# Performance work log

Measured on AMD Instinct MI355X. Metric: run time of the kernel, lower is better.

Reference implementation:

```python
import math
import jax, jax.numpy as jnp
import numpy as np

N_QUBITS = 16
BATCH = 128
N_STATE = 2 ** N_QUBITS


def cnot_ring(n_qubits):
    """Permutation equivalent to a CNOT ring (faithful copy of the torch repo's numpy code)."""
    n2 = np.array([0, 2, 3, 1])
    if n_qubits == 2:
        return n2
    evens = np.zeros(2 ** (n_qubits - 1))
    answer = n2[::2]
    for i in range(1, n_qubits - 1):
        evens[:2 ** i] = answer
        a, b = np.array_split(answer, 2)
        evens[2 ** i:2 ** i + 2 ** (i - 1)] = a + 3 * 2 ** i
        evens[2 ** i + 2 ** (i - 1):2 ** (i + 1)] = b + 2 ** i
        answer = evens[:2 ** (i + 1)]
    a, b = np.split(evens.copy() + 2 ** (n_qubits - 2), 2)
    a = np.mod(a, 2 ** (n_qubits - 1))
    b, c = np.split(b, 2)
    b = b - 2 ** (n_qubits - 1)
    odds = np.concatenate((a, b, c), axis=0)[::-1]
    output = np.zeros(2 ** n_qubits)
    output[::2] = evens
    output[1::2] = odds
    return output.astype(int)


def binary_mask(n_qubits):
    """[n, 2**n] matrix; row i is bit (n-1-i from LSB) of the column index,
    matching torch binary_matrix (dim 0 of the [2]*n tensor is the MSB)."""
    idx = jnp.arange(2 ** n_qubits, dtype=jnp.int32)
    shifts = (n_qubits - 1 - jnp.arange(n_qubits, dtype=jnp.int32))
    return ((idx[None, :] >> shifts[:, None]) & 1).astype(jnp.float32)


def wht(x):
    """Walsh-Hadamard transform over the last dim of [B, N] complex state (had_big butterfly)."""
    B, N = x.shape
    n = int(math.log2(N))
    for i in range(n):
        x = x.reshape(B, 2 ** i, 2, N >> (i + 1))
        a, b = x[:, :, 0, :], x[:, :, 1, :]
        x = jnp.stack([a + b, a - b], axis=2)
    return x.reshape(B, N) * jnp.asarray(2.0 ** (-n / 2), dtype=x.dtype)


def setup_inputs() -> dict:
    key = jax.random.key(0)
    k1, k2, k3 = jax.random.split(key, 3)
    state_re = jax.random.normal(k1, (BATCH, N_STATE), dtype=jnp.float32)
    state_im = jax.random.normal(k2, (BATCH, N_STATE), dtype=jnp.float32)
    thetas = jax.random.normal(k3, (BATCH, N_QUBITS), dtype=jnp.float32)
    cnot_p = jnp.asarray(cnot_ring(N_QUBITS), dtype=jnp.int32)
    return {"state_re": state_re, "state_im": state_im, "thetas": thetas, "cnot_p": cnot_p}


def reference(state_re, state_im, thetas, cnot_p):
    # set_state('random'): l2-normalize complex state per batch row
    norm = jnp.sqrt(jnp.sum(state_re * state_re + state_im * state_im, axis=-1, keepdims=True))
    state = (state_re + 1j * state_im) / norm  # complex64 [B, N]
    # hadamard layer (had_big WHT butterfly)
    state = wht(state)
    # RZ layer: thetas @ binary mask -> phase eigenvalues exp(-i*theta/2)
    ang = thetas @ binary_mask(N_QUBITS)  # [B, N]
    state = state * jnp.exp(-0.5j * ang)
    # CNOT ring: gather permutation over the state axis
    state = state[:, cnot_p]
    # second hadamard layer
    state = wht(state)
    # measure(): probabilities |psi|^2
    return jnp.abs(state) ** 2
```

## Files before the change

kernel.cpp:

```cpp
#include <hip/hip_runtime.h>

#define NB 128
#define NS 65536

template <int CTRL>
__device__ __forceinline__ float dppqp(float x) {
  return __int_as_float(__builtin_amdgcn_update_dpp(
      0, __float_as_int(x), CTRL, 0xF, 0xF, false));
}
template <int OFF>
__device__ __forceinline__ float dswz(float x) {
  return __int_as_float(__builtin_amdgcn_ds_swizzle(__float_as_int(x), OFF));
}

__device__ __forceinline__ void wht256(float (&xr)[4], float (&xi)[4], int lane) {
  {
    float t;
    t = xr[0]; xr[0] = t + xr[1]; xr[1] = t - xr[1];
    t = xr[2]; xr[2] = t + xr[3]; xr[3] = t - xr[3];
    t = xi[0]; xi[0] = t + xi[1]; xi[1] = t - xi[1];
    t = xi[2]; xi[2] = t + xi[3]; xi[3] = t - xi[3];
    t = xr[0]; xr[0] = t + xr[2]; xr[2] = t - xr[2];
    t = xr[1]; xr[1] = t + xr[3]; xr[3] = t - xr[3];
    t = xi[0]; xi[0] = t + xi[2]; xi[2] = t - xi[2];
    t = xi[1]; xi[1] = t + xi[3]; xi[3] = t - xi[3];
  }
  const float s1  = (lane & 1)  ? -1.f : 1.f;
  const float s2  = (lane & 2)  ? -1.f : 1.f;
  const float s4  = (lane & 4)  ? -1.f : 1.f;
  const float s8  = (lane & 8)  ? -1.f : 1.f;
  const float s16 = (lane & 16) ? -1.f : 1.f;
  const float s32 = (lane & 32) ? -1.f : 1.f;
#pragma unroll
  for (int q = 0; q < 4; ++q) {
    xr[q] = fmaf(s1, xr[q], dppqp<0xB1>(xr[q]));
    xi[q] = fmaf(s1, xi[q], dppqp<0xB1>(xi[q]));
  }
#pragma unroll
  for (int q = 0; q < 4; ++q) {
    xr[q] = fmaf(s2, xr[q], dppqp<0x4E>(xr[q]));
    xi[q] = fmaf(s2, xi[q], dppqp<0x4E>(xi[q]));
  }
#pragma unroll
  for (int q = 0; q < 4; ++q) {
    xr[q] = fmaf(s4, xr[q], dswz<0x101F>(xr[q]));
    xi[q] = fmaf(s4, xi[q], dswz<0x101F>(xi[q]));
  }
#pragma unroll
  for (int q = 0; q < 4; ++q) {
    xr[q] = fmaf(s8, xr[q], dswz<0x201F>(xr[q]));
    xi[q] = fmaf(s8, xi[q], dswz<0x201F>(xi[q]));
  }
#pragma unroll
  for (int q = 0; q < 4; ++q) {
    {
      auto r = __builtin_amdgcn_permlane16_swap(__float_as_uint(xr[q]),
                                                __float_as_uint(xr[q]), false, false);
      xr[q] = fmaf(s16, __uint_as_float(r[1]), __uint_as_float(r[0]));
    }
    {
      auto r = __builtin_amdgcn_permlane16_swap(__float_as_uint(xi[q]),
                                                __float_as_uint(xi[q]), false, false);
      xi[q] = fmaf(s16, __uint_as_float(r[1]), __uint_as_float(r[0]));
    }
  }
#pragma unroll
  for (int q = 0; q < 4; ++q) {
    {
      auto r = __builtin_amdgcn_permlane32_swap(__float_as_uint(xr[q]),
                                                __float_as_uint(xr[q]), false, false);
      xr[q] = fmaf(s32, __uint_as_float(r[1]), __uint_as_float(r[0]));
    }
    {
      auto r = __builtin_amdgcn_permlane32_swap(__float_as_uint(xi[q]),
                                                __float_as_uint(xi[q]), false, false);
      xi[q] = fmaf(s32, __uint_as_float(r[1]), __uint_as_float(r[0]));
    }
  }
}

__global__ __launch_bounds__(1024, 8) void k1_ahi(const float* __restrict__ sre,
                                                  const float* __restrict__ sim,
                                                  const float* __restrict__ thetas,
                                                  float* __restrict__ T,
                                                  float* __restrict__ partial) {
  __shared__ float sr[32][260];
  __shared__ float si[32][260];
  __shared__ float2 phh4[64];
  __shared__ float2 phHQ[4];
  __shared__ float th[16];
  __shared__ float red[16];
  const int bid = blockIdx.x;
  const int b = bid >> 3, tile = bid & 7;
  const int lo0 = tile * 32;
  const int tid = threadIdx.x, lane = tid & 63, w = tid >> 6;
  if (tid < 16) th[tid] = thetas[b * 16 + tid];
  __syncthreads();
  if (tid < 64) {
    float a = 0.f;
#pragma unroll
    for (int i = 0; i < 6; ++i)
      if ((tid >> (5 - i)) & 1) a += th[i];
    phh4[tid] = make_float2(cosf(0.5f * a), -sinf(0.5f * a));
    if (tid < 4) {
      float aq = 0.f;
      if (tid & 1) aq += th[7];
      if (tid & 2) aq += th[6];
      phHQ[tid] = make_float2(cosf(0.5f * aq), -sinf(0.5f * aq));
    }
  }
  const float* pre = sre + ((size_t)b << 16);
  const float* pim = sim + ((size_t)b << 16);
  float acc = 0.f;
  const int c = tid & 7, jr = tid >> 3;
#pragma unroll
  for (int it = 0; it < 2; ++it) {
    const int j = jr + it * 128;
    const float4 vr = *reinterpret_cast<const float4*>(pre + j * 256 + lo0 + c * 4);
    const float4 vi = *reinterpret_cast<const float4*>(pim + j * 256 + lo0 + c * 4);
    acc += vr.x*vr.x + vr.y*vr.y + vr.z*vr.z + vr.w*vr.w
         + vi.x*vi.x + vi.y*vi.y + vi.z*vi.z + vi.w*vi.w;
    sr[c*4+0][j] = vr.x; sr[c*4+1][j] = vr.y; sr[c*4+2][j] = vr.z; sr[c*4+3][j] = vr.w;
    si[c*4+0][j] = vi.x; si[c*4+1][j] = vi.y; si[c*4+2][j] = vi.z; si[c*4+3][j] = vi.w;
  }
#pragma unroll
  for (int m = 32; m >= 1; m >>= 1) acc += __shfl_xor(acc, m, 64);
  if (lane == 0) red[w] = acc;
  __syncthreads();
  if (tid == 0) {
    float sm = 0.f;
#pragma unroll
    for (int k = 0; k < 16; ++k) sm += red[k];
    partial[bid] = sm;
  }
#pragma unroll
  for (int r = 0; r < 2; ++r) {
    const int ll = w * 2 + r;
    const float4 a4 = *reinterpret_cast<const float4*>(&sr[ll][lane * 4]);
    const float4 b4 = *reinterpret_cast<const float4*>(&si[ll][lane * 4]);
    float xr[4] = {a4.x, a4.y, a4.z, a4.w};
    float xi[4] = {b4.x, b4.y, b4.z, b4.w};
    wht256(xr, xi, lane);
    const float2 p4 = phh4[lane];
#pragma unroll
    for (int q = 0; q < 4; ++q) {
      const float2 pq = phHQ[q];
      const float pr = p4.x * pq.x - p4.y * pq.y;
      const float pi = p4.x * pq.y + p4.y * pq.x;
      const float ur = xr[q], ui = xi[q];
      xr[q] = ur * pr - ui * pi;
      xi[q] = ur * pi + ui * pr;
    }
    wht256(xr, xi, lane);
    *reinterpret_cast<float4*>(&sr[ll][lane * 4]) = make_float4(xr[0], xr[1], xr[2], xr[3]);
    *reinterpret_cast<float4*>(&si[ll][lane * 4]) = make_float4(xi[0], xi[1], xi[2], xi[3]);
  }
  __syncthreads();
  float* Tb = T + ((size_t)b << 17);
  const int m = tid >> 2, sub = tid & 3;
  float* dst = Tb + ((size_t)m << 9) + (size_t)lo0 * 2;
#pragma unroll
  for (int j = 0; j < 4; ++j) {
    const int l0 = 8 * j + 2 * sub;
    *reinterpret_cast<float4*>(dst + l0 * 2) =
        make_float4(sr[l0][m], si[l0][m], sr[l0 + 1][m], si[l0 + 1][m]);
  }
}

__global__ __launch_bounds__(256, 8) void k2_alo_scatter(const float* __restrict__ T,
                                                         const float* __restrict__ thetas,
                                                         const int* __restrict__ cnot,
                                                         const float* __restrict__ partial,
                                                         float* __restrict__ outp) {
  __shared__ float2 phl4[64];
  __shared__ float2 phLQ[4];
  __shared__ int sloL[64];
  __shared__ int tj[16];
  __shared__ int srow16[16];
  __shared__ float th[16];
  __shared__ float shinv;
  const int bid = blockIdx.x;
  const int x = bid & 7, s2 = bid >> 3;
  const int b = x * 16 + (s2 >> 4), tile = s2 & 15;
  const int tid = threadIdx.x, lane = tid & 63, w = tid >> 6;
  if (tid < 16) {
    th[tid] = thetas[b * 16 + tid];
    int v = 0;
#pragma unroll
    for (int i = 0; i < 16; ++i) v |= ((cnot[1 << i] >> tid) & 1) << i;
    tj[tid] = v;
  }
  if (tid == 0) {
    float sum = 0.f;
#pragma unroll
    for (int k = 0; k < 8; ++k) sum += partial[b * 8 + k];
    shinv = 1.0f / (sum * 4294967296.0f);
  }
  __syncthreads();
  if (tid < 64) {
    float a = 0.f;
#pragma unroll
    for (int i = 0; i < 6; ++i)
      if ((tid >> (5 - i)) & 1) a += th[8 + i];
    phl4[tid] = make_float2(cosf(0.5f * a), -sinf(0.5f * a));
    int v = 0;
#pragma unroll
    for (int bb = 0; bb < 6; ++bb)
      if ((tid >> bb) & 1) v ^= tj[2 + bb];
    sloL[tid] = v;
    if (tid < 4) {
      float aq = 0.f;
      if (tid & 1) aq += th[15];
      if (tid & 2) aq += th[14];
      phLQ[tid] = make_float2(cosf(0.5f * aq), -sinf(0.5f * aq));
    }
  }
  if (tid < 16) {
    const int mh = tile * 16 + tid;
    int v = 0;
#pragma unroll
    for (int bb = 0; bb < 8; ++bb)
      if ((mh >> bb) & 1) v ^= tj[8 + bb];
    srow16[tid] = v;
  }
  __syncthreads();
  const float* Tb = T + ((size_t)b << 17);
  float* ob = outp + ((size_t)b << 16);
  const float iv = shinv;
  const float2 p4 = phl4[lane];
  const int sL = sloL[lane];
  const int sq1 = tj[0], sq2 = tj[1], sq3 = tj[0] ^ tj[1];
  float2 p4q[4];
#pragma unroll
  for (int q = 0; q < 4; ++q) {
    const float2 pq = phLQ[q];
    p4q[q].x = p4.x * pq.x - p4.y * pq.y;
    p4q[q].y = p4.x * pq.y + p4.y * pq.x;
  }
#pragma unroll
  for (int r = 0; r < 4; ++r) {
    const int rl = w * 4 + r;
    const int mh = tile * 16 + rl;
    const float4 va = *reinterpret_cast<const float4*>(Tb + ((size_t)mh << 9) + lane * 8);
    const float4 vb = *reinterpret_cast<const float4*>(Tb + ((size_t)mh << 9) + lane * 8 + 4);
    float xr[4] = {va.x, va.z, vb.x, vb.z};
    float xi[4] = {va.y, va.w, vb.y, vb.w};
    wht256(xr, xi, lane);
#pragma unroll
    for (int q = 0; q < 4; ++q) {
      const float ur = xr[q], ui = xi[q];
      xr[q] = ur * p4q[q].x - ui * p4q[q].y;
      xi[q] = ur * p4q[q].y + ui * p4q[q].x;
    }
    wht256(xr, xi, lane);
    const int base = srow16[rl] ^ sL;
    ob[base]       = (xr[0] * xr[0] + xi[0] * xi[0]) * iv;
    ob[base ^ sq1] = (xr[1] * xr[1] + xi[1] * xi[1]) * iv;
    ob[base ^ sq2] = (xr[2] * xr[2] + xi[2] * xi[2]) * iv;
    ob[base ^ sq3] = (xr[3] * xr[3] + xi[3] * xi[3]) * iv;
  }
}

extern "C" void kernel_launch(void* const* d_in, const int* in_sizes, int n_in,
                              void* d_out, int out_size, void* d_ws, size_t ws_size,
                              hipStream_t stream) {
  const float* sre = (const float*)d_in[0];
  const float* sim = (const float*)d_in[1];
  const float* thetas = (const float*)d_in[2];
  const int* cnot = (const int*)d_in[3];
  float* outp = (float*)d_out;
  char* w = (char*)d_ws;
  const size_t CPLANE = (size_t)NB * NS * 2 * sizeof(float);
  if (ws_size < CPLANE + 8192) return;
  float* T = (float*)(w);
  float* partial = (float*)(w + CPLANE);

  hipLaunchKernelGGL(k1_ahi, dim3(1024), dim3(1024), 0, stream, sre, sim, thetas, T, partial);
  hipLaunchKernelGGL(k2_alo_scatter, dim3(2048), dim3(256), 0, stream, T, thetas, cnot, partial, outp);
}
```

Measured before the change: 62.19 us.

## Load state tiles directly to LDS with XOR-swizzled layout and DPP row shuffle

The first kernel now fills LDS with global_load_lds direct-to-shared loads into an XOR-swizzled [256][32] layout, replacing register-staged float4 loads and padded transposed stores. The norm partial sum is computed from LDS reads during the butterfly pass, which removes one barrier and the separate reduction before compute. The stride-8 butterfly stage uses a DPP row_ror-style move instead of ds_swizzle. These aim to cut VGPR staging, LDS bank conflicts and LDS-pipe swizzle traffic. In exchange, the per-element LDS reads are scalar and the DPP control's correctness depends on its exact lane semantics.

```diff
diff --git a/kernel.cpp b/kernel.cpp
--- a/kernel.cpp
+++ b/kernel.cpp
@@ -3,8 +3,11 @@
 #define NB 128
 #define NS 65536
 
+typedef __attribute__((address_space(3))) float lds_float;
+typedef __attribute__((address_space(1))) const float gbl_float;
+
 template <int CTRL>
-__device__ __forceinline__ float dppqp(float x) {
+__device__ __forceinline__ float dppmov(float x) {
   return __int_as_float(__builtin_amdgcn_update_dpp(
       0, __float_as_int(x), CTRL, 0xF, 0xF, false));
 }
@@ -33,13 +36,13 @@
   const float s32 = (lane & 32) ? -1.f : 1.f;
 #pragma unroll
   for (int q = 0; q < 4; ++q) {
-    xr[q] = fmaf(s1, xr[q], dppqp<0xB1>(xr[q]));
-    xi[q] = fmaf(s1, xi[q], dppqp<0xB1>(xi[q]));
-  }
-#pragma unroll
-  for (int q = 0; q < 4; ++q) {
-    xr[q] = fmaf(s2, xr[q], dppqp<0x4E>(xr[q]));
-    xi[q] = fmaf(s2, xi[q], dppqp<0x4E>(xi[q]));
+    xr[q] = fmaf(s1, xr[q], dppmov<0xB1>(xr[q]));
+    xi[q] = fmaf(s1, xi[q], dppmov<0xB1>(xi[q]));
+  }
+#pragma unroll
+  for (int q = 0; q < 4; ++q) {
+    xr[q] = fmaf(s2, xr[q], dppmov<0x4E>(xr[q]));
+    xi[q] = fmaf(s2, xi[q], dppmov<0x4E>(xi[q]));
   }
 #pragma unroll
   for (int q = 0; q < 4; ++q) {
@@ -48,8 +51,8 @@
   }
 #pragma unroll
   for (int q = 0; q < 4; ++q) {
-    xr[q] = fmaf(s8, xr[q], dswz<0x201F>(xr[q]));
-    xi[q] = fmaf(s8, xi[q], dswz<0x201F>(xi[q]));
+    xr[q] = fmaf(s8, xr[q], dppmov<0x128>(xr[q]));
+    xi[q] = fmaf(s8, xi[q], dppmov<0x128>(xi[q]));
   }
 #pragma unroll
   for (int q = 0; q < 4; ++q) {
@@ -84,62 +87,62 @@
                                                   const float* __restrict__ thetas,
                                                   float* __restrict__ T,
                                                   float* __restrict__ partial) {
-  __shared__ float sr[32][260];
-  __shared__ float si[32][260];
+  __shared__ float SR[256][32];
+  __shared__ float SI[256][32];
   __shared__ float2 phh4[64];
   __shared__ float2 phHQ[4];
-  __shared__ float th[16];
   __shared__ float red[16];
   const int bid = blockIdx.x;
   const int b = bid >> 3, tile = bid & 7;
   const int lo0 = tile * 32;
   const int tid = threadIdx.x, lane = tid & 63, w = tid >> 6;
-  if (tid < 16) th[tid] = thetas[b * 16 + tid];
-  __syncthreads();
+  const float* pre = sre + ((size_t)b << 16);
+  const float* pim = sim + ((size_t)b << 16);
+
+  {
+    const float* src = (w < 8) ? pre : pim;
+    float* dst0 = (w < 8) ? &SR[0][0] : &SI[0][0];
+    const int w8 = w & 7;
+    const int cl = lane & 31, half = lane >> 5;
+#pragma unroll
+    for (int i = 0; i < 16; ++i) {
+      const int jb = w8 * 32 + i * 2;
+      const int s = (jb >> 2) & 31;
+      const float* gp = src + (jb + half) * 256 + lo0 + (cl ^ s);
+      __builtin_amdgcn_global_load_lds((gbl_float*)gp,
+                                       (lds_float*)(dst0 + jb * 32), 4, 0, 0);
+    }
+  }
   if (tid < 64) {
+    const float* tb = thetas + b * 16;
     float a = 0.f;
 #pragma unroll
     for (int i = 0; i < 6; ++i)
-      if ((tid >> (5 - i)) & 1) a += th[i];
+      if ((tid >> (5 - i)) & 1) a += tb[i];
     phh4[tid] = make_float2(cosf(0.5f * a), -sinf(0.5f * a));
     if (tid < 4) {
       float aq = 0.f;
-      if (tid & 1) aq += th[7];
-      if (tid & 2) aq += th[6];
+      if (tid & 1) aq += tb[7];
+      if (tid & 2) aq += tb[6];
       phHQ[tid] = make_float2(cosf(0.5f * aq), -sinf(0.5f * aq));
     }
   }
-  const float* pre = sre + ((size_t)b << 16);
-  const float* pim = sim + ((size_t)b << 16);
+  __syncthreads();
+
   float acc = 0.f;
-  const int c = tid & 7, jr = tid >> 3;
-#pragma unroll
-  for (int it = 0; it < 2; ++it) {
-    const int j = jr + it * 128;
-    const float4 vr = *reinterpret_cast<const float4*>(pre + j * 256 + lo0 + c * 4);
-    const float4 vi = *reinterpret_cast<const float4*>(pim + j * 256 + lo0 + c * 4);
-    acc += vr.x*vr.x + vr.y*vr.y + vr.z*vr.z + vr.w*vr.w
-         + vi.x*vi.x + vi.y*vi.y + vi.z*vi.z + vi.w*vi.w;
-    sr[c*4+0][j] = vr.x; sr[c*4+1][j] = vr.y; sr[c*4+2][j] = vr.z; sr[c*4+3][j] = vr.w;
-    si[c*4+0][j] = vi.x; si[c*4+1][j] = vi.y; si[c*4+2][j] = vi.z; si[c*4+3][j] = vi.w;
-  }
-#pragma unroll
-  for (int m = 32; m >= 1; m >>= 1) acc += __shfl_xor(acc, m, 64);
-  if (lane == 0) red[w] = acc;
-  __syncthreads();
-  if (tid == 0) {
-    float sm = 0.f;
-#pragma unroll
-    for (int k = 0; k < 16; ++k) sm += red[k];
-    partial[bid] = sm;
-  }
+  const int sw = lane & 31;
 #pragma unroll
   for (int r = 0; r < 2; ++r) {
     const int ll = w * 2 + r;
-    const float4 a4 = *reinterpret_cast<const float4*>(&sr[ll][lane * 4]);
-    const float4 b4 = *reinterpret_cast<const float4*>(&si[ll][lane * 4]);
-    float xr[4] = {a4.x, a4.y, a4.z, a4.w};
-    float xi[4] = {b4.x, b4.y, b4.z, b4.w};
+    const int col = ll ^ sw;
+    float xr[4], xi[4];
+#pragma unroll
+    for (int q = 0; q < 4; ++q) {
+      xr[q] = SR[4 * lane + q][col];
+      xi[q] = SI[4 * lane + q][col];
+    }
+    acc += xr[0]*xr[0]+xr[1]*xr[1]+xr[2]*xr[2]+xr[3]*xr[3]
+         + xi[0]*xi[0]+xi[1]*xi[1]+xi[2]*xi[2]+xi[3]*xi[3];
     wht256(xr, xi, lane);
     const float2 p4 = phh4[lane];
 #pragma unroll
@@ -152,18 +155,35 @@
       xi[q] = ur * pi + ui * pr;
     }
     wht256(xr, xi, lane);
-    *reinterpret_cast<float4*>(&sr[ll][lane * 4]) = make_float4(xr[0], xr[1], xr[2], xr[3]);
-    *reinterpret_cast<float4*>(&si[ll][lane * 4]) = make_float4(xi[0], xi[1], xi[2], xi[3]);
-  }
+#pragma unroll
+    for (int q = 0; q < 4; ++q) {
+      SR[4 * lane + q][col] = xr[q];
+      SI[4 * lane + q][col] = xi[q];
+    }
+  }
+#pragma unroll
+  for (int m = 32; m >= 1; m >>= 1) acc += __shfl_xor(acc, m, 64);
+  if (lane == 0) red[w] = acc;
   __syncthreads();
+  if (tid == 0) {
+    float sm = 0.f;
+#pragma unroll
+    for (int k = 0; k < 16; ++k) sm += red[k];
+    partial[bid] = sm;
+  }
   float* Tb = T + ((size_t)b << 17);
-  const int m = tid >> 2, sub = tid & 3;
-  float* dst = Tb + ((size_t)m << 9) + (size_t)lo0 * 2;
-#pragma unroll
-  for (int j = 0; j < 4; ++j) {
-    const int l0 = 8 * j + 2 * sub;
-    *reinterpret_cast<float4*>(dst + l0 * 2) =
-        make_float4(sr[l0][m], si[l0][m], sr[l0 + 1][m], si[l0 + 1][m]);
+  const int chunk = tid & 7;
+#pragma unroll
+  for (int it = 0; it < 2; ++it) {
+    const int m = (tid >> 3) + it * 128;
+    const int s = (m >> 2) & 31;
+    const int c0 = (4 * chunk) ^ s, c1 = (4 * chunk + 1) ^ s,
+              c2 = (4 * chunk + 2) ^ s, c3 = (4 * chunk + 3) ^ s;
+    float* dst = Tb + ((size_t)m << 9) + (size_t)(lo0 + 4 * chunk) * 2;
+    *reinterpret_cast<float4*>(dst) =
+        make_float4(SR[m][c0], SI[m][c0], SR[m][c1], SI[m][c1]);
+    *reinterpret_cast<float4*>(dst + 4) =
+        make_float4(SR[m][c2], SI[m][c2], SR[m][c3], SI[m][c3]);
   }
 }
 
```

New measurement: 68.39 us. +10.0%, slower.
